# Optimization experiments

Hardware: AMD Instinct MI355X
Metric: run time of the kernel (lower is better)

Reference implementation:

```python
import jax, jax.numpy as jnp
import numpy as np

D = 512          # d_model
DS = 32          # d_state
EXPAND = 2
HEADDIM = 64
R = 4            # mimo_rank
DIN = EXPAND * D             # 1024 inner dim
H = DIN // HEADDIM           # 16 heads
DFF = ((int(D * 8 / 3) + 7) // 8) * 8  # 1368 SwiGLU hidden
CHUNK = max(1, 64 // R)      # 16
BATCH, SEQ = 4, 512


def setup_inputs() -> dict:
    key = jax.random.key(0)
    ks = jax.random.split(key, 12)
    def w(k, shape, fan):
        return jax.random.normal(k, shape, jnp.float32) / np.float32(np.sqrt(fan))
    return {
        "x": jax.random.normal(ks[0], (BATCH, SEQ, D), jnp.float32),
        "mask": jnp.ones((BATCH, SEQ), jnp.float32),
        "norm1_w": jnp.ones((D,), jnp.float32),
        "norm2_w": jnp.ones((D,), jnp.float32),
        "Wz": w(ks[1], (D, DIN), D),
        "Wx": w(ks[2], (D, DIN), D),
        "Wb": w(ks[3], (D, H * R * DS), D),
        "Wc": w(ks[4], (D, H * R * DS), D),
        "Wdt": w(ks[5], (D, H), D),
        "dt_bias": jnp.zeros((H,), jnp.float32),
        "A_log": jnp.log(jnp.arange(1, H + 1, dtype=jnp.float32)),
        "D_skip": jnp.ones((H,), jnp.float32),
        "Wout": w(ks[6], (DIN, D), DIN),
        "w1": w(ks[7], (D, DFF), D),
        "w2": w(ks[8], (DFF, D), DFF),
        "w3": w(ks[9], (D, DFF), D),
    }


def rmsnorm(x, wgt, eps=1e-6):
    rms = jnp.sqrt(jnp.mean(x * x, axis=-1, keepdims=True) + eps)
    return x / rms * wgt


def ssm_mixer(x, Wz, Wx, Wb, Wc, Wdt, dt_bias, A_log, D_skip, Wout):
    # x: [B, S, D] (already masked)
    B, S, _ = x.shape
    pad = (CHUNK - S % CHUNK) % CHUNK
    if pad > 0:
        x = jnp.pad(x, ((0, 0), (0, pad), (0, 0)))
    Sp = x.shape[1]
    z = x @ Wz                                        # [B,Sp,DIN] gate
    u = (x @ Wx).reshape(B, Sp, H, HEADDIM)           # [B,Sp,H,P]
    Bm = (x @ Wb).reshape(B, Sp, H, R, DS)            # [B,Sp,H,R,N]
    Cm = (x @ Wc).reshape(B, Sp, H, R, DS)
    dt = jax.nn.softplus(x @ Wdt + dt_bias)           # [B,Sp,H]
    a = jnp.exp(dt * (-jnp.exp(A_log)))               # per-step decay [B,Sp,H]
    ud = u * dt[..., None]                            # discretized input

    def step(h, inp):
        a_t, B_t, C_t, ud_t = inp                     # [B,H], [B,H,R,N], [B,H,R,N], [B,H,P]
        h = a_t[:, :, None, None, None] * h + jnp.einsum('bhrn,bhp->bhrnp', B_t, ud_t)
        y = jnp.einsum('bhrn,bhrnp->bhp', C_t, h)
        return h, y

    h0 = jnp.zeros((B, H, R, DS, HEADDIM), x.dtype)
    xs = (a.swapaxes(0, 1), Bm.swapaxes(0, 1), Cm.swapaxes(0, 1), ud.swapaxes(0, 1))
    _, ys = jax.lax.scan(step, h0, xs)                # ys: [Sp,B,H,P]
    y = ys.swapaxes(0, 1) + u * D_skip[None, None, :, None]
    y = y.reshape(B, Sp, DIN) * jax.nn.silu(z)
    y = y @ Wout                                      # [B,Sp,D]
    return y[:, :S]


def reference(x, mask, norm1_w, norm2_w, Wz, Wx, Wb, Wc, Wdt, dt_bias,
              A_log, D_skip, Wout, w1, w2, w3):
    m = mask[..., None]
    xn = rmsnorm(x, norm1_w) * m
    y = ssm_mixer(xn, Wz, Wx, Wb, Wc, Wdt, dt_bias, A_log, D_skip, Wout) * m
    x = x + y
    xn2 = rmsnorm(x, norm2_w)
    x = x + (jax.nn.silu(xn2 @ w1) * (xn2 @ w3)) @ w2
    return x * m
```

## Files before the change

kernel.cpp:

```cpp
#include <hip/hip_runtime.h>
#include <hip/hip_bf16.h>
#include <math.h>

#define Bn 4
#define Sn 512
#define Dn 512
#define DINn 1024
#define Hn 16
#define Pn 64
#define RNn 128
#define DFFn 1368
#define KP2 1408
#define BSn (Bn*Sn)
#define CH 64
#define NCH (Sn/CH)
#define PSTR 6144
#define FPAD 2816
#define NSCAN (Bn*NCH*Hn)
#define NRMS 512

typedef __attribute__((ext_vector_type(8))) short short8;
typedef __attribute__((ext_vector_type(4))) float f32x4;
typedef __attribute__((ext_vector_type(4))) short short4v;

static __device__ __forceinline__ float bf2f(__hip_bfloat16 v){return __bfloat162float(v);}
static __device__ __forceinline__ __hip_bfloat16 f2bf(float v){return __float2bfloat16(v);}
static __device__ __forceinline__ short f2bfs(float v){ __hip_bfloat16 b=f2bf(v); short s; __builtin_memcpy(&s,&b,2); return s; }
static __device__ __forceinline__ float bfs2f(short s){ __hip_bfloat16 b; __builtin_memcpy(&b,&s,2); return bf2f(b); }

static __device__ __forceinline__ int xcd_swz(int bid, int q) {
  return (bid & 7) * q + (bid >> 3);
}

typedef const __attribute__((address_space(1))) unsigned int* gas1_u32p;
typedef __attribute__((address_space(3))) unsigned int* gas3_u32p;
static __device__ __forceinline__ void gl_lds16(const void* g, void* l) {
  __builtin_amdgcn_global_load_lds((gas1_u32p)g, (gas3_u32p)l, 16, 0, 0);
}

struct T8 {
  const float* src[8];
  const float* svec[8];
  __hip_bfloat16* dst[8];
  int Rr[8], Cc[8], RrPad[8], CcPad[8], gw[8];
  int start[9];
};

static __device__ __forceinline__ void transpose_tile(const T8& d, int bid, int t,
                                                      float (*tile)[65]) {
  int i = 0;
#pragma unroll
  for (int k = 1; k < 8; ++k) if (bid >= d.start[k]) i = k;
  int rel = bid - d.start[i];
  int gx = rel % d.gw[i], gy = rel / d.gw[i];
  const float* in = d.src[i];
  const float* sv = d.svec[i];
  __hip_bfloat16* out = d.dst[i];
  int Rr = d.Rr[i], Cc = d.Cc[i], RrPad = d.RrPad[i], CcPad = d.CcPad[i];
  int tx = t & 15, ty = t >> 4;
#pragma unroll
  for (int i4 = 0; i4 < 4; ++i4) {
    int r = gy * 64 + ty + i4 * 16;
    int c0 = gx * 64 + tx * 4;
    f32x4 v = (f32x4){0.f, 0.f, 0.f, 0.f};
    if (r < Rr && c0 + 3 < Cc) v = *(const f32x4*)(in + (size_t)r * Cc + c0);
    tile[ty + i4 * 16][tx * 4 + 0] = v[0];
    tile[ty + i4 * 16][tx * 4 + 1] = v[1];
    tile[ty + i4 * 16][tx * 4 + 2] = v[2];
    tile[ty + i4 * 16][tx * 4 + 3] = v[3];
  }
  __syncthreads();
#pragma unroll
  for (int i4 = 0; i4 < 4; ++i4) {
    int r2 = gx * 64 + ty + i4 * 16;
    int c2 = gy * 64 + tx * 4;
    if (r2 < CcPad && c2 + 3 < RrPad) {
      int k = ty + i4 * 16;
      float s0 = sv ? sv[c2 + 0] : 1.f;
      float s1 = sv ? sv[c2 + 1] : 1.f;
      float s2 = sv ? sv[c2 + 2] : 1.f;
      float s3 = sv ? sv[c2 + 3] : 1.f;
      short4v o;
      o.x = f2bfs(tile[tx * 4 + 0][k] * s0);
      o.y = f2bfs(tile[tx * 4 + 1][k] * s1);
      o.z = f2bfs(tile[tx * 4 + 2][k] * s2);
      o.w = f2bfs(tile[tx * 4 + 3][k] * s3);
      *(short4v*)((short*)out + (size_t)r2 * RrPad + c2) = o;
    }
  }
}

__global__ __launch_bounds__(256) void prep_kernel(
    T8 d, const float* __restrict__ x, const float* __restrict__ w,
    const float* __restrict__ mask, const float* __restrict__ Wdt,
    const float* __restrict__ dtb, const float* __restrict__ Alog,
    __hip_bfloat16* __restrict__ outb, float* __restrict__ dt,
    float* __restrict__ la, float* __restrict__ rs, int tstart) {
  __shared__ __align__(16) char smem[40960];
  int bid = blockIdx.x, t = threadIdx.x;
  if (bid < tstart) {
    transpose_tile(d, bid, t, (float(*)[65])smem);
  } else if (bid - tstart < NRMS) {
    float* wdtS = (float*)smem;
    float* xsS  = (float*)(smem + 32768);
#pragma unroll
    for (int i = 0; i < 8; ++i) {
      int idx = t + i * 256;
      *(f32x4*)&wdtS[idx * 4] = *(const f32x4*)&Wdt[idx * 4];
    }
    __syncthreads();
    int wv = t >> 6, lane = t & 63;
    int row = (bid - tstart) * 4 + wv;
    const float* xr = x + (size_t)row * Dn;
    f32x4 v0 = *(const f32x4*)(xr + lane * 4);
    f32x4 v1 = *(const f32x4*)(xr + 256 + lane * 4);
    float ss = v0[0]*v0[0] + v0[1]*v0[1] + v0[2]*v0[2] + v0[3]*v0[3]
             + v1[0]*v1[0] + v1[1]*v1[1] + v1[2]*v1[2] + v1[3]*v1[3];
#pragma unroll
    for (int o = 32; o > 0; o >>= 1) ss += __shfl_xor(ss, o);
    float sc = rsqrtf(ss * (1.f / Dn) + 1e-6f) * mask[row];
    f32x4 w0 = *(const f32x4*)(w + lane * 4);
    f32x4 w1 = *(const f32x4*)(w + 256 + lane * 4);
    f32x4 o0, o1;
#pragma unroll
    for (int j = 0; j < 4; ++j) { o0[j] = v0[j] * sc * w0[j]; o1[j] = v1[j] * sc * w1[j]; }
    short4v b0, b1;
    b0.x = f2bfs(o0[0]); b0.y = f2bfs(o0[1]); b0.z = f2bfs(o0[2]); b0.w = f2bfs(o0[3]);
    b1.x = f2bfs(o1[0]); b1.y = f2bfs(o1[1]); b1.z = f2bfs(o1[2]); b1.w = f2bfs(o1[3]);
    *(short4v*)((short*)outb + (size_t)row * Dn + lane * 4) = b0;
    *(short4v*)((short*)outb + (size_t)row * Dn + 256 + lane * 4) = b1;
    *(f32x4*)&xsS[wv * 512 + lane * 4] = o0;
    *(f32x4*)&xsS[wv * 512 + 256 + lane * 4] = o1;
    int h = lane >> 2, j = lane & 3;
    float s = 0.f;
#pragma unroll 8
    for (int kk = 0; kk < 128; ++kk) {
      int k = j + kk * 4;
      s = fmaf(xsS[wv * 512 + k], wdtS[k * Hn + h], s);
    }
    s += __shfl_down(s, 2, 4);
    s += __shfl_down(s, 1, 4);
    if (j == 0) {
      float v = s + dtb[h];
      float sp = (v > 20.f) ? v : log1pf(expf(v));
      float Ah = expf(Alog[h]);
      dt[(size_t)row * Hn + h] = sp;
      la[(size_t)row * Hn + h] = -Ah * sp;
    }
  } else {
    *(f32x4*)&rs[t * 8]     = (f32x4){0.f, 0.f, 0.f, 0.f};
    *(f32x4*)&rs[t * 8 + 4] = (f32x4){0.f, 0.f, 0.f, 0.f};
  }
}

__global__ __launch_bounds__(256) void gemm_kernel(
    const __hip_bfloat16* __restrict__ A, const __hip_bfloat16* __restrict__ BT,
    __hip_bfloat16* __restrict__ C, int M, int N, int K) {
  __shared__ short As[2][4096];
  __shared__ short Bs[2][4096];
  int mblocks = M >> 7;
  int wg = xcd_swz(blockIdx.x, (int)gridDim.x >> 3);
  int m0 = (wg % mblocks) * 128, n0 = (wg / mblocks) * 128;
  int t = threadIdx.x;
  int lane = t & 63, wv = t >> 6;
  int wm = (wv & 1) * 64, wn = (wv >> 1) * 64;
  f32x4 acc[4][4];
#pragma unroll
  for (int i = 0; i < 4; ++i)
#pragma unroll
    for (int j = 0; j < 4; ++j) acc[i][j] = (f32x4){0.f, 0.f, 0.f, 0.f};
  const short* Ag = (const short*)A;
  const short* Bg = (const short*)BT;
  int r0 = t >> 2, p = t & 3;
  int q0 = (p - (r0 >> 1)) & 3;
  int r1 = r0 + 64;
  int q1 = (p - (r1 >> 1)) & 3;
  const short* Asrc0 = Ag + (size_t)(m0 + r0) * K + 8 * q0;
  const short* Asrc1 = Ag + (size_t)(m0 + r1) * K + 8 * q1;
  const short* Bsrc0 = Bg + (size_t)(n0 + r0) * K + 8 * q0;
  const short* Bsrc1 = Bg + (size_t)(n0 + r1) * K + 8 * q1;
  int fr = lane & 15, fq = lane >> 4;
  int kTiles = K >> 5;
  auto stage = [&](int buf, int k0) {
    gl_lds16(Asrc0 + k0, &As[buf][wv * 512]);
    gl_lds16(Asrc1 + k0, &As[buf][2048 + wv * 512]);
    gl_lds16(Bsrc0 + k0, &Bs[buf][wv * 512]);
    gl_lds16(Bsrc1 + k0, &Bs[buf][2048 + wv * 512]);
  };
  auto domfma = [&](int buf) {
    short8 af[4], bfr[4];
#pragma unroll
    for (int i = 0; i < 4; ++i) {
      int rr = wm + i * 16 + fr;
      af[i] = *(const short8*)&As[buf][rr * 32 + (((rr >> 1) + fq) & 3) * 8];
    }
#pragma unroll
    for (int i = 0; i < 4; ++i) {
      int rr = wn + i * 16 + fr;
      bfr[i] = *(const short8*)&Bs[buf][rr * 32 + (((rr >> 1) + fq) & 3) * 8];
    }
#pragma unroll
    for (int mi = 0; mi < 4; ++mi)
#pragma unroll
      for (int ni = 0; ni < 4; ++ni)
        acc[mi][ni] = __builtin_amdgcn_mfma_f32_16x16x32_bf16(af[mi], bfr[ni], acc[mi][ni], 0, 0, 0);
  };
  stage(0, 0);
  for (int kt = 0; kt < kTiles; ++kt) {
    int buf = kt & 1;
    __syncthreads();
    if (kt + 1 < kTiles) stage(buf ^ 1, (kt + 1) << 5);
    domfma(buf);
  }
  int fq4 = (lane >> 4) * 4;
#pragma unroll
  for (int mi = 0; mi < 4; ++mi)
#pragma unroll
    for (int ni = 0; ni < 4; ++ni) {
      int col = n0 + wn + ni * 16 + fr;
      if (col < N) {
        int rowb = m0 + wm + mi * 16 + fq4;
#pragma unroll
        for (int r = 0; r < 4; ++r)
          C[(size_t)(rowb + r) * N + col] = f2bf(acc[mi][ni][r]);
      }
    }
}

template <int MODE>
__global__ __launch_bounds__(256) void gemm64_ep_kernel(
    const __hip_bfloat16* __restrict__ A, const __hip_bfloat16* __restrict__ BT,
    const float* __restrict__ aux, const float* __restrict__ mask,
    float* __restrict__ out, __hip_bfloat16* __restrict__ outb,
    float* __restrict__ rs, int M, int N, int K) {
  __shared__ short As[2][64][72];
  __shared__ short Bs[2][64][72];
  int mblocks = M >> 6;
  int wg = xcd_swz(blockIdx.x, (int)gridDim.x >> 3);
  int m0 = (wg % mblocks) * 64, n0 = (wg / mblocks) * 64;
  int t = threadIdx.x;
  int lane = t & 63, wv = t >> 6;
  int wm = (wv & 1) * 32, wn = (wv >> 1) * 32;
  f32x4 acc[2][2];
#pragma unroll
  for (int i = 0; i < 2; ++i)
#pragma unroll
    for (int j = 0; j < 2; ++j) acc[i][j] = (f32x4){0.f, 0.f, 0.f, 0.f};
  const short* Ag = (const short*)A;
  const short* Bg = (const short*)BT;
  int sr = t >> 2;
  int sc = (t & 3) * 16;
  const short* Ap = Ag + (size_t)(m0 + sr) * K + sc;
  const short* Bp = Bg + (size_t)(n0 + sr) * K + sc;
  int fr = lane & 15, fq = (lane >> 4) * 8;
  int kTiles = K >> 6;
  short8 a0A = 0, a1A = 0, b0A = 0, b1A = 0;
  short8 a0B = 0, a1B = 0, b0B = 0, b1B = 0;
  auto loadA = [&](int k0) {
    a0A = *(const short8*)(Ap + k0);
    a1A = *(const short8*)(Ap + k0 + 8);
    b0A = *(const short8*)(Bp + k0);
    b1A = *(const short8*)(Bp + k0 + 8);
  };
  auto loadB = [&](int k0) {
    a0B = *(const short8*)(Ap + k0);
    a1B = *(const short8*)(Ap + k0 + 8);
    b0B = *(const short8*)(Bp + k0);
    b1B = *(const short8*)(Bp + k0 + 8);
  };
  auto storeA = [&](int buf) {
    *(short8*)&As[buf][sr][sc] = a0A;
    *(short8*)&As[buf][sr][sc + 8] = a1A;
    *(short8*)&Bs[buf][sr][sc] = b0A;
    *(short8*)&Bs[buf][sr][sc + 8] = b1A;
  };
  auto storeB = [&](int buf) {
    *(short8*)&As[buf][sr][sc] = a0B;
    *(short8*)&As[buf][sr][sc + 8] = a1B;
    *(short8*)&Bs[buf][sr][sc] = b0B;
    *(short8*)&Bs[buf][sr][sc + 8] = b1B;
  };
  auto mfma = [&](int buf) {
#pragma unroll
    for (int kk = 0; kk < 2; ++kk) {
      short8 af[2], bfr[2];
#pragma unroll
      for (int i = 0; i < 2; ++i) af[i] = *(const short8*)&As[buf][wm + i * 16 + fr][kk * 32 + fq];
#pragma unroll
      for (int i = 0; i < 2; ++i) bfr[i] = *(const short8*)&Bs[buf][wn + i * 16 + fr][kk * 32 + fq];
#pragma unroll
      for (int mi = 0; mi < 2; ++mi)
#pragma unroll
        for (int ni = 0; ni < 2; ++ni)
          acc[mi][ni] = __builtin_amdgcn_mfma_f32_16x16x32_bf16(af[mi], bfr[ni], acc[mi][ni], 0, 0, 0);
    }
  };
  loadA(0);
  storeA(0);
  loadA(64);
  __syncthreads();
  for (int kt = 0; kt < kTiles; kt += 2) {
    storeA(1);
    if (kt + 2 < kTiles) loadB((kt + 2) << 6);
    mfma(0);
    __syncthreads();
    if (kt + 2 < kTiles) storeB(0);
    if (kt + 3 < kTiles) loadA((kt + 3) << 6);
    mfma(1);
    __syncthreads();
  }
  int fq4 = (lane >> 4) * 4;
  float rsum[2][4];
#pragma unroll
  for (int mi = 0; mi < 2; ++mi)
#pragma unroll
    for (int r = 0; r < 4; ++r) rsum[mi][r] = 0.f;
#pragma unroll
  for (int mi = 0; mi < 2; ++mi)
#pragma unroll
    for (int ni = 0; ni < 2; ++ni) {
      int col = n0 + wn + ni * 16 + fr;
#pragma unroll
      for (int r = 0; r < 4; ++r) {
        int row = m0 + wm + mi * 16 + fq4 + r;
        float m = mask[row];
        size_t a = (size_t)row * N + col;
        float v = acc[mi][ni][r];
        if (MODE == 1) {
          float ov = aux[a] + v * m;
          out[a] = ov;
          outb[a] = f2bf(ov);
          rsum[mi][r] += ov * ov;
        } else {
          out[a] = (aux[a] + v) * m;
        }
      }
    }
  if (MODE == 1) {
#pragma unroll
    for (int mi = 0; mi < 2; ++mi)
#pragma unroll
      for (int r = 0; r < 4; ++r) {
        float s = rsum[mi][r];
#pragma unroll
        for (int o = 8; o > 0; o >>= 1) s += __shfl_xor(s, o);
        if ((lane & 15) == 0) {
          int row = m0 + wm + mi * 16 + fq4 + r;
          atomicAdd(&rs[row], s);
        }
      }
  }
}

__global__ __launch_bounds__(256) void gemm64g_kernel(
    const __hip_bfloat16* __restrict__ A, const float* __restrict__ rs,
    const __hip_bfloat16* __restrict__ BT, __hip_bfloat16* __restrict__ G,
    int M, int K) {
  __shared__ short As[2][64][72];
  __shared__ short B1s[2][64][72];
  __shared__ short B3s[2][64][72];
  __shared__ float ssc[64];
  int mblocks = M >> 6;
  int wg = xcd_swz(blockIdx.x, (int)gridDim.x >> 3);
  int m0 = (wg % mblocks) * 64, n0 = (wg / mblocks) * 64;
  int t = threadIdx.x;
  int lane = t & 63, wv = t >> 6;
  int wm = (wv & 1) * 32, wn = (wv >> 1) * 32;
  f32x4 acc1[2][2], acc3[2][2];
#pragma unroll
  for (int i = 0; i < 2; ++i)
#pragma unroll
    for (int j = 0; j < 2; ++j) {
      acc1[i][j] = (f32x4){0.f, 0.f, 0.f, 0.f};
      acc3[i][j] = (f32x4){0.f, 0.f, 0.f, 0.f};
    }
  const short* Ag = (const short*)A;
  const short* Bg = (const short*)BT;
  int sr = t >> 2;
  int sc = (t & 3) * 16;
  const short* Ap  = Ag + (size_t)(m0 + sr) * K + sc;
  const short* B1p = Bg + (size_t)(n0 + sr) * K + sc;
  const short* B3p = Bg + (size_t)(DFFn + n0 + sr) * K + sc;
  int fr = lane & 15, fq = (lane >> 4) * 8;
  int kTiles = K >> 6;
  if (t < 64) ssc[t] = rsqrtf(rs[m0 + t] * (1.f / Dn) + 1e-6f);
  short8 a0A = 0, a1A = 0, c0A = 0, c1A = 0, d0A = 0, d1A = 0;
  short8 a0B = 0, a1B = 0, c0B = 0, c1B = 0, d0B = 0, d1B = 0;
  auto loadA = [&](int k0) {
    a0A = *(const short8*)(Ap + k0);
    a1A = *(const short8*)(Ap + k0 + 8);
    c0A = *(const short8*)(B1p + k0);
    c1A = *(const short8*)(B1p + k0 + 8);
    d0A = *(const short8*)(B3p + k0);
    d1A = *(const short8*)(B3p + k0 + 8);
  };
  auto loadB = [&](int k0) {
    a0B = *(const short8*)(Ap + k0);
    a1B = *(const short8*)(Ap + k0 + 8);
    c0B = *(const short8*)(B1p + k0);
    c1B = *(const short8*)(B1p + k0 + 8);
    d0B = *(const short8*)(B3p + k0);
    d1B = *(const short8*)(B3p + k0 + 8);
  };
  auto storeA = [&](int buf) {
    *(short8*)&As[buf][sr][sc] = a0A;
    *(short8*)&As[buf][sr][sc + 8] = a1A;
    *(short8*)&B1s[buf][sr][sc] = c0A;
    *(short8*)&B1s[buf][sr][sc + 8] = c1A;
    *(short8*)&B3s[buf][sr][sc] = d0A;
    *(short8*)&B3s[buf][sr][sc + 8] = d1A;
  };
  auto storeB = [&](int buf) {
    *(short8*)&As[buf][sr][sc] = a0B;
    *(short8*)&As[buf][sr][sc + 8] = a1B;
    *(short8*)&B1s[buf][sr][sc] = c0B;
    *(short8*)&B1s[buf][sr][sc + 8] = c1B;
    *(short8*)&B3s[buf][sr][sc] = d0B;
    *(short8*)&B3s[buf][sr][sc + 8] = d1B;
  };
  auto mfma = [&](int buf) {
#pragma unroll
    for (int kk = 0; kk < 2; ++kk) {
      short8 af[2], b1f[2], b3f[2];
#pragma unroll
      for (int i = 0; i < 2; ++i) af[i]  = *(const short8*)&As[buf][wm + i * 16 + fr][kk * 32 + fq];
#pragma unroll
      for (int i = 0; i < 2; ++i) b1f[i] = *(const short8*)&B1s[buf][wn + i * 16 + fr][kk * 32 + fq];
#pragma unroll
      for (int i = 0; i < 2; ++i) b3f[i] = *(const short8*)&B3s[buf][wn + i * 16 + fr][kk * 32 + fq];
#pragma unroll
      for (int mi = 0; mi < 2; ++mi)
#pragma unroll
        for (int ni = 0; ni < 2; ++ni) {
          acc1[mi][ni] = __builtin_amdgcn_mfma_f32_16x16x32_bf16(af[mi], b1f[ni], acc1[mi][ni], 0, 0, 0);
          acc3[mi][ni] = __builtin_amdgcn_mfma_f32_16x16x32_bf16(af[mi], b3f[ni], acc3[mi][ni], 0, 0, 0);
        }
    }
  };
  loadA(0);
  storeA(0);
  loadA(64);
  __syncthreads();
  for (int kt = 0; kt < kTiles; kt += 2) {
    storeA(1);
    if (kt + 2 < kTiles) loadB((kt + 2) << 6);
    mfma(0);
    __syncthreads();
    if (kt + 2 < kTiles) storeB(0);
    if (kt + 3 < kTiles) loadA((kt + 3) << 6);
    mfma(1);
    __syncthreads();
  }
  int fq4 = (lane >> 4) * 4;
#pragma unroll
  for (int mi = 0; mi < 2; ++mi)
#pragma unroll
    for (int ni = 0; ni < 2; ++ni) {
      int col = n0 + wn + ni * 16 + fr;
      bool valid = col < DFFn;
#pragma unroll
      for (int r = 0; r < 4; ++r) {
        int rloc = wm + mi * 16 + fq4 + r;
        float scl = ssc[rloc];
        float h1v = acc1[mi][ni][r] * scl;
        float sil = h1v / (1.f + __expf(-h1v));
        float g = sil * (acc3[mi][ni][r] * scl);
        G[(size_t)(m0 + rloc) * KP2 + col] = valid ? f2bf(g) : f2bf(0.f);
      }
    }
}

__global__ __launch_bounds__(256) void chunk_intra_kernel(
    const __hip_bfloat16* __restrict__ P, const float* __restrict__ dt,
    const float* __restrict__ la, __hip_bfloat16* __restrict__ ysb,
    __hip_bfloat16* __restrict__ Sbuf, float* __restrict__ ecL, float* __restrict__ ec) {
  int id = blockIdx.x;
  int h = id & 15, c = (id >> 4) & 7, b = id >> 7;
  int t = threadIdx.x, lane = t & 63, wv = t >> 6;
  __shared__ __align__(16) char smem[55040];
  short* sCB = (short*)smem;
  short* sB  = (short*)(smem + 18432);
  short* sUD = (short*)(smem + 35840);
  short* sG  = (short*)(smem + 45056);
  float* scum = (float*)(smem + 54272);
  float* sws  = scum + 64;
  float* sdt  = sws + 64;
  int row0 = b * Sn + c * CH;
  const short* Pb = (const short*)P;
#pragma unroll
  for (int i = 0; i < 4; ++i) {
    int idx = t + i * 256;
    int r = idx >> 4, kk = (idx & 15) * 8;
    *(short8*)&sCB[r * 136 + kk] = *(const short8*)(Pb + (size_t)(row0 + r) * PSTR + 4096 + h * 128 + kk);
    *(short8*)&sB [r * 136 + kk] = *(const short8*)(Pb + (size_t)(row0 + r) * PSTR + 2048 + h * 128 + kk);
  }
  if (t < 64) { sdt[t] = dt[(size_t)(row0 + t) * Hn + h]; scum[t] = la[(size_t)(row0 + t) * Hn + h]; }
  __syncthreads();
  if (wv == 0) {
    float v = scum[lane];
#pragma unroll
    for (int o = 1; o < 64; o <<= 1) { float n = __shfl_up(v, o); if (lane >= o) v += n; }
    scum[lane] = v;
    float c63 = __shfl(v, 63);
    sws[lane] = __expf(c63 - v);
    ec[((size_t)((b * NCH + c) * Hn + h)) * 64 + lane] = __expf(v);
    if (lane == 0) ecL[(b * NCH + c) * Hn + h] = __expf(c63);
  }
#pragma unroll
  for (int i = 0; i < 2; ++i) {
    int idx = t + i * 256;
    int s = idx >> 3, pc = (idx & 7) * 8;
    short8 uv = *(const short8*)(Pb + (size_t)(row0 + s) * PSTR + 1024 + h * 64 + pc);
    float dv = sdt[s];
#pragma unroll
    for (int j = 0; j < 8; ++j) sUD[(pc + j) * 72 + s] = f2bfs(bfs2f(uv[j]) * dv);
  }
  __syncthreads();
  int fr = lane & 15, fq = (lane >> 4) * 8, q4 = (lane >> 4) * 4;
  {
    short8 af[4];
#pragma unroll
    for (int k = 0; k < 4; ++k) af[k] = *(short8*)&sCB[(16 * wv + fr) * 136 + k * 32 + fq];
#pragma unroll
    for (int j = 0; j < 4; ++j) {
      f32x4 acc = (f32x4){0.f, 0.f, 0.f, 0.f};
#pragma unroll
      for (int k = 0; k < 4; ++k) {
        short8 bf = *(short8*)&sB[(16 * j + fr) * 136 + k * 32 + fq];
        acc = __builtin_amdgcn_mfma_f32_16x16x32_bf16(af[k], bf, acc, 0, 0, 0);
      }
      int ss = 16 * j + fr;
      float cs = scum[ss];
#pragma unroll
      for (int r = 0; r < 4; ++r) {
        int tt = 16 * wv + q4 + r;
        float w = (ss <= tt) ? __expf(scum[tt] - cs) : 0.f;
        sG[tt * 72 + ss] = f2bfs(acc[r] * w);
      }
    }
  }
  __syncthreads();
#pragma unroll
  for (int i = 0; i < 32; ++i) {
    int idx = t + i * 256;
    int rn = idx >> 6, s = idx & 63;
    sCB[rn * 72 + s] = f2bfs(bfs2f(sB[s * 136 + rn]) * sws[s]);
  }
  __syncthreads();
  {
    short8 ag[2];
#pragma unroll
    for (int k = 0; k < 2; ++k) ag[k] = *(short8*)&sG[(16 * wv + fr) * 72 + k * 32 + fq];
#pragma unroll
    for (int j = 0; j < 4; ++j) {
      f32x4 acc = (f32x4){0.f, 0.f, 0.f, 0.f};
#pragma unroll
      for (int k = 0; k < 2; ++k) {
        short8 bf = *(short8*)&sUD[(16 * j + fr) * 72 + k * 32 + fq];
        acc = __builtin_amdgcn_mfma_f32_16x16x32_bf16(ag[k], bf, acc, 0, 0, 0);
      }
#pragma unroll
      for (int r = 0; r < 4; ++r)
        ysb[(size_t)(row0 + 16 * wv + q4 + r) * DINn + h * 64 + 16 * j + fr] = f2bf(acc[r]);
    }
  }
#pragma unroll
  for (int mt0 = 0; mt0 < 2; ++mt0) {
    int mt = wv * 2 + mt0;
    short8 ab[2];
#pragma unroll
    for (int k = 0; k < 2; ++k) ab[k] = *(short8*)&sCB[(16 * mt + fr) * 72 + k * 32 + fq];
#pragma unroll
    for (int j = 0; j < 4; ++j) {
      f32x4 acc = (f32x4){0.f, 0.f, 0.f, 0.f};
#pragma unroll
      for (int k = 0; k < 2; ++k) {
        short8 bf = *(short8*)&sUD[(16 * j + fr) * 72 + k * 32 + fq];
        acc = __builtin_amdgcn_mfma_f32_16x16x32_bf16(ab[k], bf, acc, 0, 0, 0);
      }
      int pp = 16 * j + fr;
      int rn0 = 16 * mt + q4;
      short4v o;
      o.x = f2bfs(acc[0]); o.y = f2bfs(acc[1]); o.z = f2bfs(acc[2]); o.w = f2bfs(acc[3]);
      *(short4v*)&((short*)Sbuf)[((size_t)((b * NCH + c) * Hn + h) * 64 + pp) * 128 + rn0] = o;
    }
  }
}

__global__ __launch_bounds__(256) void inter_gate_kernel(
    const __hip_bfloat16* __restrict__ P, const __hip_bfloat16* __restrict__ Sbuf,
    const float* __restrict__ ecL, const float* __restrict__ ec,
    const __hip_bfloat16* __restrict__ ysb, const float* __restrict__ Dsk,
    __hip_bfloat16* __restrict__ y2b) {
  int id = blockIdx.x;
  int h = id & 15, c = (id >> 4) & 7, b = id >> 7;
  int t = threadIdx.x, lane = t & 63, wv = t >> 6;
  __shared__ __align__(16) short sC[64 * 136];
  __shared__ __align__(16) short sHt[64 * 136];
  __shared__ __align__(16) short sz[64 * 64];
  __shared__ __align__(16) short su[64 * 64];
  __shared__ float sec[64];
  int row0 = b * Sn + c * CH;
  const short* Pb = (const short*)P;
#pragma unroll
  for (int i = 0; i < 2; ++i) {
    int idx = t + i * 256;
    int r = idx >> 3, pc = (idx & 7) * 8;
    *(short8*)&sz[r * 64 + pc] = *(const short8*)(Pb + (size_t)(row0 + r) * PSTR + h * 64 + pc);
    *(short8*)&su[r * 64 + pc] = *(const short8*)(Pb + (size_t)(row0 + r) * PSTR + 1024 + h * 64 + pc);
  }
  if (c > 0) {
#pragma unroll
    for (int i = 0; i < 4; ++i) {
      int idx = t + i * 256;
      int r = idx >> 4, kk = (idx & 15) * 8;
      *(short8*)&sC[r * 136 + kk] = *(const short8*)(Pb + (size_t)(row0 + r) * PSTR + 4096 + h * 128 + kk);
    }
    float hacc[32];
#pragma unroll
    for (int jj = 0; jj < 32; ++jj) hacc[jj] = 0.f;
    const short* Sb = (const short*)Sbuf;
    float wrun = 1.f;
    for (int cp = c - 1; cp >= 0; --cp) {
      size_t base = ((size_t)((b * NCH + cp) * Hn + h)) * 8192 + (size_t)t * 32;
#pragma unroll
      for (int v4 = 0; v4 < 4; ++v4) {
        short8 sv = *(const short8*)(Sb + base + v4 * 8);
#pragma unroll
        for (int jj = 0; jj < 8; ++jj)
          hacc[v4 * 8 + jj] = fmaf(wrun, bfs2f(sv[jj]), hacc[v4 * 8 + jj]);
      }
      wrun *= ecL[(size_t)((b * NCH + cp) * Hn + h)];
    }
    int p = t >> 2, rn0 = (t & 3) * 32;
#pragma unroll
    for (int v4 = 0; v4 < 4; ++v4) {
      short8 o;
#pragma unroll
      for (int jj = 0; jj < 8; ++jj) o[jj] = f2bfs(hacc[v4 * 8 + jj]);
      *(short8*)&sHt[p * 136 + rn0 + v4 * 8] = o;
    }
    if (t < 64) sec[t] = ec[((size_t)((b * NCH + c) * Hn + h)) * 64 + t];
  }
  __syncthreads();
  int fr = lane & 15, fq = (lane >> 4) * 8, q4 = (lane >> 4) * 4;
  f32x4 acc[4];
#pragma unroll
  for (int j = 0; j < 4; ++j) acc[j] = (f32x4){0.f, 0.f, 0.f, 0.f};
  if (c > 0) {
    short8 af[4];
#pragma unroll
    for (int k = 0; k < 4; ++k) af[k] = *(short8*)&sC[(16 * wv + fr) * 136 + k * 32 + fq];
#pragma unroll
    for (int j = 0; j < 4; ++j)
#pragma unroll
      for (int k = 0; k < 4; ++k) {
        short8 bf = *(short8*)&sHt[(16 * j + fr) * 136 + k * 32 + fq];
        acc[j] = __builtin_amdgcn_mfma_f32_16x16x32_bf16(af[k], bf, acc[j], 0, 0, 0);
      }
  }
  float dsk = Dsk[h];
#pragma unroll
  for (int j = 0; j < 4; ++j) {
    int col = 16 * j + fr;
#pragma unroll
    for (int r = 0; r < 4; ++r) {
      int tt = 16 * wv + q4 + r;
      size_t a = (size_t)(row0 + tt) * DINn + h * 64 + col;
      float val = bf2f(ysb[a]);
      if (c > 0) val += sec[tt] * acc[j][r];
      float uu = bfs2f(su[tt * 64 + col]);
      float zz = bfs2f(sz[tt * 64 + col]);
      float sil = zz / (1.f + __expf(-zz));
      y2b[a] = f2bf((val + uu * dsk) * sil);
    }
  }
}

extern "C" void kernel_launch(void* const* d_in, const int* in_sizes, int n_in,
                              void* d_out, int out_size, void* d_ws, size_t ws_size,
                              hipStream_t stream) {
  const float* x    = (const float*)d_in[0];
  const float* mask = (const float*)d_in[1];
  const float* n1w  = (const float*)d_in[2];
  const float* n2w  = (const float*)d_in[3];
  const float* Wz   = (const float*)d_in[4];
  const float* Wx   = (const float*)d_in[5];
  const float* Wb   = (const float*)d_in[6];
  const float* Wc   = (const float*)d_in[7];
  const float* Wdt  = (const float*)d_in[8];
  const float* dtb  = (const float*)d_in[9];
  const float* Alog = (const float*)d_in[10];
  const float* Dsk  = (const float*)d_in[11];
  const float* Wout = (const float*)d_in[12];
  const float* w1   = (const float*)d_in[13];
  const float* w2   = (const float*)d_in[14];
  const float* w3   = (const float*)d_in[15];

  char* ws = (char*)d_ws;
  size_t off = 0;
  auto alloc = [&](size_t bytes) {
    char* p = ws + off;
    off += (bytes + 255) & ~(size_t)255;
    return p;
  };
  __hip_bfloat16* xnb = (__hip_bfloat16*)alloc((size_t)BSn * Dn * 2);
  __hip_bfloat16* P = (__hip_bfloat16*)alloc((size_t)BSn * PSTR * 2);
  float* dt  = (float*)alloc((size_t)BSn * Hn * 4);
  float* la  = (float*)alloc((size_t)BSn * Hn * 4);
  __hip_bfloat16* ysb = (__hip_bfloat16*)alloc((size_t)BSn * DINn * 2);
  float* ecL = (float*)alloc((size_t)Bn * NCH * Hn * 4);
  float* ec  = (float*)alloc((size_t)Bn * NCH * Hn * 64 * 4);
  float* rs  = (float*)alloc((size_t)BSn * 4);
  __hip_bfloat16* WallT = (__hip_bfloat16*)alloc((size_t)PSTR * Dn * 2);
  __hip_bfloat16* WoutT = (__hip_bfloat16*)alloc((size_t)Dn * DINn * 2);
  __hip_bfloat16* w13T  = (__hip_bfloat16*)alloc((size_t)FPAD * Dn * 2);
  __hip_bfloat16* w2T   = (__hip_bfloat16*)alloc((size_t)Dn * KP2 * 2);
  char* arena = alloc(23200000);
  __hip_bfloat16* Sbuf = (__hip_bfloat16*)arena;
  __hip_bfloat16* y2b  = (__hip_bfloat16*)(arena + 16777216);
  float* xres          = (float*)arena;
  __hip_bfloat16* gatedb = (__hip_bfloat16*)(arena + 4194304);
  __hip_bfloat16* xresb  = (__hip_bfloat16*)(arena + 20971520);

  T8 td;
  for (int i = 0; i < 8; ++i) td.svec[i] = nullptr;
  td.src[0] = Wz;   td.dst[0] = WallT;                      td.Rr[0] = 512;  td.Cc[0] = 1024; td.RrPad[0] = 512;  td.CcPad[0] = 1024;
  td.src[1] = Wx;   td.dst[1] = WallT + (size_t)1024 * 512; td.Rr[1] = 512;  td.Cc[1] = 1024; td.RrPad[1] = 512;  td.CcPad[1] = 1024;
  td.src[2] = Wb;   td.dst[2] = WallT + (size_t)2048 * 512; td.Rr[2] = 512;  td.Cc[2] = 2048; td.RrPad[2] = 512;  td.CcPad[2] = 2048;
  td.src[3] = Wc;   td.dst[3] = WallT + (size_t)4096 * 512; td.Rr[3] = 512;  td.Cc[3] = 2048; td.RrPad[3] = 512;  td.CcPad[3] = 2048;
  td.src[4] = Wout; td.dst[4] = WoutT;                      td.Rr[4] = 1024; td.Cc[4] = 512;  td.RrPad[4] = 1024; td.CcPad[4] = 512;
  td.src[5] = w1;   td.dst[5] = w13T;                       td.Rr[5] = 512;  td.Cc[5] = 1368; td.RrPad[5] = 512;  td.CcPad[5] = 1368;
  td.src[6] = w3;   td.dst[6] = w13T + (size_t)1368 * 512;  td.Rr[6] = 512;  td.Cc[6] = 1368; td.RrPad[6] = 512;  td.CcPad[6] = 1448;
  td.src[7] = w2;   td.dst[7] = w2T;                        td.Rr[7] = 1368; td.Cc[7] = 512;  td.RrPad[7] = KP2;  td.CcPad[7] = 512;
  td.svec[5] = n2w;
  td.svec[6] = n2w;
  int tot = 0;
  for (int i = 0; i < 8; ++i) {
    td.gw[i] = (td.CcPad[i] + 63) / 64;
    int gh = (td.RrPad[i] + 63) / 64;
    td.start[i] = tot;
    tot += td.gw[i] * gh;
  }
  td.start[8] = tot;

  prep_kernel<<<tot + NRMS + 1, 256, 0, stream>>>(td, x, n1w, mask, Wdt, dtb, Alog, xnb, dt, la, rs, tot);
  gemm_kernel<<<16 * 48, 256, 0, stream>>>(xnb, WallT, P, BSn, PSTR, Dn);
  chunk_intra_kernel<<<NSCAN, 256, 0, stream>>>(P, dt, la, ysb, Sbuf, ecL, ec);
  inter_gate_kernel<<<NSCAN, 256, 0, stream>>>(P, Sbuf, ecL, ec, ysb, Dsk, y2b);
  gemm64_ep_kernel<1><<<32 * 8, 256, 0, stream>>>(y2b, WoutT, x, mask, xres, xresb, rs, BSn, Dn, DINn);
  gemm64g_kernel<<<32 * (KP2 / 64), 256, 0, stream>>>(xresb, rs, w13T, gatedb, BSn, Dn);
  gemm64_ep_kernel<2><<<32 * 8, 256, 0, stream>>>(gatedb, w2T, xres, mask, (float*)d_out, nullptr, rs, BSn, Dn, KP2);
}
```

Measured before the change: 187.0 us.

## Switch post-scan GEMMs to 128x128 tiles with direct global-to-LDS swizzled loads

Measured after the change: 224.6 us. +20.1%, slower.

```diff
diff --git a/kernel.cpp b/kernel.cpp
--- a/kernel.cpp
+++ b/kernel.cpp
@@ -228,97 +228,77 @@
 }
 
 template <int MODE>
-__global__ __launch_bounds__(256) void gemm64_ep_kernel(
+__global__ __launch_bounds__(256) void gemm128_ep_kernel(
     const __hip_bfloat16* __restrict__ A, const __hip_bfloat16* __restrict__ BT,
     const float* __restrict__ aux, const float* __restrict__ mask,
     float* __restrict__ out, __hip_bfloat16* __restrict__ outb,
     float* __restrict__ rs, int M, int N, int K) {
-  __shared__ short As[2][64][72];
-  __shared__ short Bs[2][64][72];
-  int mblocks = M >> 6;
+  __shared__ short As[2][4096];
+  __shared__ short Bs[2][4096];
+  int mblocks = M >> 7;
   int wg = xcd_swz(blockIdx.x, (int)gridDim.x >> 3);
-  int m0 = (wg % mblocks) * 64, n0 = (wg / mblocks) * 64;
+  int m0 = (wg % mblocks) * 128, n0 = (wg / mblocks) * 128;
   int t = threadIdx.x;
   int lane = t & 63, wv = t >> 6;
-  int wm = (wv & 1) * 32, wn = (wv >> 1) * 32;
-  f32x4 acc[2][2];
-#pragma unroll
-  for (int i = 0; i < 2; ++i)
-#pragma unroll
-    for (int j = 0; j < 2; ++j) acc[i][j] = (f32x4){0.f, 0.f, 0.f, 0.f};
+  int wm = (wv & 1) * 64, wn = (wv >> 1) * 64;
+  f32x4 acc[4][4];
+#pragma unroll
+  for (int i = 0; i < 4; ++i)
+#pragma unroll
+    for (int j = 0; j < 4; ++j) acc[i][j] = (f32x4){0.f, 0.f, 0.f, 0.f};
   const short* Ag = (const short*)A;
   const short* Bg = (const short*)BT;
-  int sr = t >> 2;
-  int sc = (t & 3) * 16;
-  const short* Ap = Ag + (size_t)(m0 + sr) * K + sc;
-  const short* Bp = Bg + (size_t)(n0 + sr) * K + sc;
-  int fr = lane & 15, fq = (lane >> 4) * 8;
-  int kTiles = K >> 6;
-  short8 a0A = 0, a1A = 0, b0A = 0, b1A = 0;
-  short8 a0B = 0, a1B = 0, b0B = 0, b1B = 0;
-  auto loadA = [&](int k0) {
-    a0A = *(const short8*)(Ap + k0);
-    a1A = *(const short8*)(Ap + k0 + 8);
-    b0A = *(const short8*)(Bp + k0);
-    b1A = *(const short8*)(Bp + k0 + 8);
+  int r0 = t >> 2, p = t & 3;
+  int q0 = (p - (r0 >> 1)) & 3;
+  int r1 = r0 + 64;
+  int q1 = (p - (r1 >> 1)) & 3;
+  const short* Asrc0 = Ag + (size_t)(m0 + r0) * K + 8 * q0;
+  const short* Asrc1 = Ag + (size_t)(m0 + r1) * K + 8 * q1;
+  const short* Bsrc0 = Bg + (size_t)(n0 + r0) * K + 8 * q0;
+  const short* Bsrc1 = Bg + (size_t)(n0 + r1) * K + 8 * q1;
+  int fr = lane & 15, fq = lane >> 4;
+  int kTiles = K >> 5;
+  auto stage = [&](int buf, int k0) {
+    gl_lds16(Asrc0 + k0, &As[buf][wv * 512]);
+    gl_lds16(Asrc1 + k0, &As[buf][2048 + wv * 512]);
+    gl_lds16(Bsrc0 + k0, &Bs[buf][wv * 512]);
+    gl_lds16(Bsrc1 + k0, &Bs[buf][2048 + wv * 512]);
   };
-  auto loadB = [&](int k0) {
-    a0B = *(const short8*)(Ap + k0);
-    a1B = *(const short8*)(Ap + k0 + 8);
-    b0B = *(const short8*)(Bp + k0);
-    b1B = *(const short8*)(Bp + k0 + 8);
+  auto domfma = [&](int buf) {
+    short8 af[4], bfr[4];
+#pragma unroll
+    for (int i = 0; i < 4; ++i) {
+      int rr = wm + i * 16 + fr;
+      af[i] = *(const short8*)&As[buf][rr * 32 + (((rr >> 1) + fq) & 3) * 8];
+    }
+#pragma unroll
+    for (int i = 0; i < 4; ++i) {
+      int rr = wn + i * 16 + fr;
+      bfr[i] = *(const short8*)&Bs[buf][rr * 32 + (((rr >> 1) + fq) & 3) * 8];
+    }
+#pragma unroll
+    for (int mi = 0; mi < 4; ++mi)
+#pragma unroll
+      for (int ni = 0; ni < 4; ++ni)
+        acc[mi][ni] = __builtin_amdgcn_mfma_f32_16x16x32_bf16(af[mi], bfr[ni], acc[mi][ni], 0, 0, 0);
   };
-  auto storeA = [&](int buf) {
-    *(short8*)&As[buf][sr][sc] = a0A;
-    *(short8*)&As[buf][sr][sc + 8] = a1A;
-    *(short8*)&Bs[buf][sr][sc] = b0A;
-    *(short8*)&Bs[buf][sr][sc + 8] = b1A;
-  };
-  auto storeB = [&](int buf) {
-    *(short8*)&As[buf][sr][sc] = a0B;
-    *(short8*)&As[buf][sr][sc + 8] = a1B;
-    *(short8*)&Bs[buf][sr][sc] = b0B;
-    *(short8*)&Bs[buf][sr][sc + 8] = b1B;
-  };
-  auto mfma = [&](int buf) {
-#pragma unroll
-    for (int kk = 0; kk < 2; ++kk) {
-      short8 af[2], bfr[2];
-#pragma unroll
-      for (int i = 0; i < 2; ++i) af[i] = *(const short8*)&As[buf][wm + i * 16 + fr][kk * 32 + fq];
-#pragma unroll
-      for (int i = 0; i < 2; ++i) bfr[i] = *(const short8*)&Bs[buf][wn + i * 16 + fr][kk * 32 + fq];
-#pragma unroll
-      for (int mi = 0; mi < 2; ++mi)
-#pragma unroll
-        for (int ni = 0; ni < 2; ++ni)
-          acc[mi][ni] = __builtin_amdgcn_mfma_f32_16x16x32_bf16(af[mi], bfr[ni], acc[mi][ni], 0, 0, 0);
-    }
-  };
-  loadA(0);
-  storeA(0);
-  loadA(64);
-  __syncthreads();
-  for (int kt = 0; kt < kTiles; kt += 2) {
-    storeA(1);
-    if (kt + 2 < kTiles) loadB((kt + 2) << 6);
-    mfma(0);
+  stage(0, 0);
+  for (int kt = 0; kt < kTiles; ++kt) {
+    int buf = kt & 1;
     __syncthreads();
-    if (kt + 2 < kTiles) storeB(0);
-    if (kt + 3 < kTiles) loadA((kt + 3) << 6);
-    mfma(1);
-    __syncthreads();
+    if (kt + 1 < kTiles) stage(buf ^ 1, (kt + 1) << 5);
+    domfma(buf);
   }
   int fq4 = (lane >> 4) * 4;
-  float rsum[2][4];
-#pragma unroll
-  for (int mi = 0; mi < 2; ++mi)
+  float rsum[4][4];
+#pragma unroll
+  for (int mi = 0; mi < 4; ++mi)
 #pragma unroll
     for (int r = 0; r < 4; ++r) rsum[mi][r] = 0.f;
 #pragma unroll
-  for (int mi = 0; mi < 2; ++mi)
-#pragma unroll
-    for (int ni = 0; ni < 2; ++ni) {
+  for (int mi = 0; mi < 4; ++mi)
+#pragma unroll
+    for (int ni = 0; ni < 4; ++ni) {
       int col = n0 + wn + ni * 16 + fr;
 #pragma unroll
       for (int r = 0; r < 4; ++r) {
@@ -338,7 +318,7 @@
     }
   if (MODE == 1) {
 #pragma unroll
-    for (int mi = 0; mi < 2; ++mi)
+    for (int mi = 0; mi < 4; ++mi)
 #pragma unroll
       for (int r = 0; r < 4; ++r) {
         float s = rsum[mi][r];
@@ -352,112 +332,86 @@
   }
 }
 
-__global__ __launch_bounds__(256) void gemm64g_kernel(
+__global__ __launch_bounds__(256) void gemm128g_kernel(
     const __hip_bfloat16* __restrict__ A, const float* __restrict__ rs,
     const __hip_bfloat16* __restrict__ BT, __hip_bfloat16* __restrict__ G,
     int M, int K) {
-  __shared__ short As[2][64][72];
-  __shared__ short B1s[2][64][72];
-  __shared__ short B3s[2][64][72];
-  __shared__ float ssc[64];
-  int mblocks = M >> 6;
+  __shared__ short As[2][4096];
+  __shared__ short B1s[2][4096];
+  __shared__ short B3s[2][4096];
+  __shared__ float ssc[128];
+  int mblocks = M >> 7;
   int wg = xcd_swz(blockIdx.x, (int)gridDim.x >> 3);
-  int m0 = (wg % mblocks) * 64, n0 = (wg / mblocks) * 64;
+  int m0 = (wg % mblocks) * 128, n0 = (wg / mblocks) * 128;
   int t = threadIdx.x;
   int lane = t & 63, wv = t >> 6;
-  int wm = (wv & 1) * 32, wn = (wv >> 1) * 32;
-  f32x4 acc1[2][2], acc3[2][2];
-#pragma unroll
-  for (int i = 0; i < 2; ++i)
-#pragma unroll
-    for (int j = 0; j < 2; ++j) {
+  int wm = (wv & 1) * 64, wn = (wv >> 1) * 64;
+  f32x4 acc1[4][4], acc3[4][4];
+#pragma unroll
+  for (int i = 0; i < 4; ++i)
+#pragma unroll
+    for (int j = 0; j < 4; ++j) {
       acc1[i][j] = (f32x4){0.f, 0.f, 0.f, 0.f};
       acc3[i][j] = (f32x4){0.f, 0.f, 0.f, 0.f};
     }
   const short* Ag = (const short*)A;
   const short* Bg = (const short*)BT;
-  int sr = t >> 2;
-  int sc = (t & 3) * 16;
-  const short* Ap  = Ag + (size_t)(m0 + sr) * K + sc;
-  const short* B1p = Bg + (size_t)(n0 + sr) * K + sc;
-  const short* B3p = Bg + (size_t)(DFFn + n0 + sr) * K + sc;
-  int fr = lane & 15, fq = (lane >> 4) * 8;
-  int kTiles = K >> 6;
-  if (t < 64) ssc[t] = rsqrtf(rs[m0 + t] * (1.f / Dn) + 1e-6f);
-  short8 a0A = 0, a1A = 0, c0A = 0, c1A = 0, d0A = 0, d1A = 0;
-  short8 a0B = 0, a1B = 0, c0B = 0, c1B = 0, d0B = 0, d1B = 0;
-  auto loadA = [&](int k0) {
-    a0A = *(const short8*)(Ap + k0);
-    a1A = *(const short8*)(Ap + k0 + 8);
-    c0A = *(const short8*)(B1p + k0);
-    c1A = *(const short8*)(B1p + k0 + 8);
-    d0A = *(const short8*)(B3p + k0);
-    d1A = *(const short8*)(B3p + k0 + 8);
+  int r0 = t >> 2, p = t & 3;
+  int q0 = (p - (r0 >> 1)) & 3;
+  int r1 = r0 + 64;
+  int q1 = (p - (r1 >> 1)) & 3;
+  const short* Asrc0  = Ag + (size_t)(m0 + r0) * K + 8 * q0;
+  const short* Asrc1  = Ag + (size_t)(m0 + r1) * K + 8 * q1;
+  const short* B1src0 = Bg + (size_t)(n0 + r0) * K + 8 * q0;
+  const short* B1src1 = Bg + (size_t)(n0 + r1) * K + 8 * q1;
+  const short* B3src0 = Bg + (size_t)(KP2 + n0 + r0) * K + 8 * q0;
+  const short* B3src1 = Bg + (size_t)(KP2 + n0 + r1) * K + 8 * q1;
+  int fr = lane & 15, fq = lane >> 4;
+  int kTiles = K >> 5;
+  if (t < 128) ssc[t] = rsqrtf(rs[m0 + t] * (1.f / Dn) + 1e-6f);
+  auto stage = [&](int buf, int k0) {
+    gl_lds16(Asrc0 + k0, &As[buf][wv * 512]);
+    gl_lds16(Asrc1 + k0, &As[buf][2048 + wv * 512]);
+    gl_lds16(B1src0 + k0, &B1s[buf][wv * 512]);
+    gl_lds16(B1src1 + k0, &B1s[buf][2048 + wv * 512]);
+    gl_lds16(B3src0 + k0, &B3s[buf][wv * 512]);
+    gl_lds16(B3src1 + k0, &B3s[buf][2048 + wv * 512]);
   };
-  auto loadB = [&](int k0) {
-    a0B = *(const short8*)(Ap + k0);
-    a1B = *(const short8*)(Ap + k0 + 8);
-    c0B = *(const short8*)(B1p + k0);
-    c1B = *(const short8*)(B1p + k0 + 8);
-    d0B = *(const short8*)(B3p + k0);
-    d1B = *(const short8*)(B3p + k0 + 8);
+  auto domfma = [&](int buf) {
+    short8 af[4], b1f[4], b3f[4];
+#pragma unroll
+    for (int i = 0; i < 4; ++i) {
+      int rr = wm + i * 16 + fr;
+      af[i] = *(const short8*)&As[buf][rr * 32 + (((rr >> 1) + fq) & 3) * 8];
+    }
+#pragma unroll
+    for (int i = 0; i < 4; ++i) {
+      int rr = wn + i * 16 + fr;
+      int so = rr * 32 + (((rr >> 1) + fq) & 3) * 8;
+      b1f[i] = *(const short8*)&B1s[buf][so];
+      b3f[i] = *(const short8*)&B3s[buf][so];
+    }
+#pragma unroll
+    for (int mi = 0; mi < 4; ++mi)
+#pragma unroll
+      for (int ni = 0; ni < 4; ++ni) {
+        acc1[mi][ni] = __builtin_amdgcn_mfma_f32_16x16x32_bf16(af[mi], b1f[ni], acc1[mi][ni], 0, 0, 0);
+        acc3[mi][ni] = __builtin_amdgcn_mfma_f32_16x16x32_bf16(af[mi], b3f[ni], acc3[mi][ni], 0, 0, 0);
+      }
   };
-  auto storeA = [&](int buf) {
-    *(short8*)&As[buf][sr][sc] = a0A;
-    *(short8*)&As[buf][sr][sc + 8] = a1A;
-    *(short8*)&B1s[buf][sr][sc] = c0A;
-    *(short8*)&B1s[buf][sr][sc + 8] = c1A;
-    *(short8*)&B3s[buf][sr][sc] = d0A;
-    *(short8*)&B3s[buf][sr][sc + 8] = d1A;
-  };
-  auto storeB = [&](int buf) {
-    *(short8*)&As[buf][sr][sc] = a0B;
-    *(short8*)&As[buf][sr][sc + 8] = a1B;
-    *(short8*)&B1s[buf][sr][sc] = c0B;
-    *(short8*)&B1s[buf][sr][sc + 8] = c1B;
-    *(short8*)&B3s[buf][sr][sc] = d0B;
-    *(short8*)&B3s[buf][sr][sc + 8] = d1B;
-  };
-  auto mfma = [&](int buf) {
-#pragma unroll
-    for (int kk = 0; kk < 2; ++kk) {
-      short8 af[2], b1f[2], b3f[2];
-#pragma unroll
-      for (int i = 0; i < 2; ++i) af[i]  = *(const short8*)&As[buf][wm + i * 16 + fr][kk * 32 + fq];
-#pragma unroll
-      for (int i = 0; i < 2; ++i) b1f[i] = *(const short8*)&B1s[buf][wn + i * 16 + fr][kk * 32 + fq];
-#pragma unroll
-      for (int i = 0; i < 2; ++i) b3f[i] = *(const short8*)&B3s[buf][wn + i * 16 + fr][kk * 32 + fq];
-#pragma unroll
-      for (int mi = 0; mi < 2; ++mi)
-#pragma unroll
-        for (int ni = 0; ni < 2; ++ni) {
-          acc1[mi][ni] = __builtin_amdgcn_mfma_f32_16x16x32_bf16(af[mi], b1f[ni], acc1[mi][ni], 0, 0, 0);
-          acc3[mi][ni] = __builtin_amdgcn_mfma_f32_16x16x32_bf16(af[mi], b3f[ni], acc3[mi][ni], 0, 0, 0);
-        }
-    }
-  };
-  loadA(0);
-  storeA(0);
-  loadA(64);
-  __syncthreads();
-  for (int kt = 0; kt < kTiles; kt += 2) {
-    storeA(1);
-    if (kt + 2 < kTiles) loadB((kt + 2) << 6);
-    mfma(0);
+  stage(0, 0);
+  for (int kt = 0; kt < kTiles; ++kt) {
+    int buf = kt & 1;
     __syncthreads();
-    if (kt + 2 < kTiles) storeB(0);
-    if (kt + 3 < kTiles) loadA((kt + 3) << 6);
-    mfma(1);
-    __syncthreads();
+    if (kt + 1 < kTiles) stage(buf ^ 1, (kt + 1) << 5);
+    domfma(buf);
   }
   int fq4 = (lane >> 4) * 4;
 #pragma unroll
-  for (int mi = 0; mi < 2; ++mi)
-#pragma unroll
-    for (int ni = 0; ni < 2; ++ni) {
+  for (int mi = 0; mi < 4; ++mi)
+#pragma unroll
+    for (int ni = 0; ni < 4; ++ni) {
       int col = n0 + wn + ni * 16 + fr;
-      bool valid = col < DFFn;
 #pragma unroll
       for (int r = 0; r < 4; ++r) {
         int rloc = wm + mi * 16 + fq4 + r;
@@ -465,7 +419,7 @@
         float h1v = acc1[mi][ni][r] * scl;
         float sil = h1v / (1.f + __expf(-h1v));
         float g = sil * (acc3[mi][ni][r] * scl);
-        G[(size_t)(m0 + rloc) * KP2 + col] = valid ? f2bf(g) : f2bf(0.f);
+        G[(size_t)(m0 + rloc) * KP2 + col] = f2bf(g);
       }
     }
 }
@@ -730,8 +684,8 @@
   td.src[2] = Wb;   td.dst[2] = WallT + (size_t)2048 * 512; td.Rr[2] = 512;  td.Cc[2] = 2048; td.RrPad[2] = 512;  td.CcPad[2] = 2048;
   td.src[3] = Wc;   td.dst[3] = WallT + (size_t)4096 * 512; td.Rr[3] = 512;  td.Cc[3] = 2048; td.RrPad[3] = 512;  td.CcPad[3] = 2048;
   td.src[4] = Wout; td.dst[4] = WoutT;                      td.Rr[4] = 1024; td.Cc[4] = 512;  td.RrPad[4] = 1024; td.CcPad[4] = 512;
-  td.src[5] = w1;   td.dst[5] = w13T;                       td.Rr[5] = 512;  td.Cc[5] = 1368; td.RrPad[5] = 512;  td.CcPad[5] = 1368;
-  td.src[6] = w3;   td.dst[6] = w13T + (size_t)1368 * 512;  td.Rr[6] = 512;  td.Cc[6] = 1368; td.RrPad[6] = 512;  td.CcPad[6] = 1448;
+  td.src[5] = w1;   td.dst[5] = w13T;                       td.Rr[5] = 512;  td.Cc[5] = 1368; td.RrPad[5] = 512;  td.CcPad[5] = KP2;
+  td.src[6] = w3;   td.dst[6] = w13T + (size_t)KP2 * 512;   td.Rr[6] = 512;  td.Cc[6] = 1368; td.RrPad[6] = 512;  td.CcPad[6] = KP2;
   td.src[7] = w2;   td.dst[7] = w2T;                        td.Rr[7] = 1368; td.Cc[7] = 512;  td.RrPad[7] = KP2;  td.CcPad[7] = 512;
   td.svec[5] = n2w;
   td.svec[6] = n2w;
@@ -748,7 +702,7 @@
   gemm_kernel<<<16 * 48, 256, 0, stream>>>(xnb, WallT, P, BSn, PSTR, Dn);
   chunk_intra_kernel<<<NSCAN, 256, 0, stream>>>(P, dt, la, ysb, Sbuf, ecL, ec);
   inter_gate_kernel<<<NSCAN, 256, 0, stream>>>(P, Sbuf, ecL, ec, ysb, Dsk, y2b);
-  gemm64_ep_kernel<1><<<32 * 8, 256, 0, stream>>>(y2b, WoutT, x, mask, xres, xresb, rs, BSn, Dn, DINn);
-  gemm64g_kernel<<<32 * (KP2 / 64), 256, 0, stream>>>(xresb, rs, w13T, gatedb, BSn, Dn);
-  gemm64_ep_kernel<2><<<32 * 8, 256, 0, stream>>>(gatedb, w2T, xres, mask, (float*)d_out, nullptr, rs, BSn, Dn, KP2);
-}
+  gemm128_ep_kernel<1><<<16 * 4, 256, 0, stream>>>(y2b, WoutT, x, mask, xres, xresb, rs, BSn, Dn, DINn);
+  gemm128g_kernel<<<16 * (KP2 / 128), 256, 0, stream>>>(xresb, rs, w13T, gatedb, BSn, Dn);
+  gemm128_ep_kernel<2><<<16 * 4, 256, 0, stream>>>(gatedb, w2T, xres, mask, (float*)d_out, nullptr, rs, BSn, Dn, KP2);
+}
```
